# Kernel optimization log

Hardware: AMD Instinct MI355X
Metric: run time of the kernel (lower is better)

Reference implementation:

```python
import jax, jax.numpy as jnp
import numpy as np

WINDOW = 8
HEADS = 8

def _rel_index(w):
    coords = np.stack(np.meshgrid(np.arange(w), np.arange(w), indexing='ij')).reshape(2, -1)
    rel = coords[:, :, None] - coords[:, None, :]          # [2, N, N]
    rel = rel.transpose(1, 2, 0) + (w - 1)                 # [N, N, 2]
    return jnp.asarray(rel[:, :, 0] * (2 * w - 1) + rel[:, :, 1])  # [N, N] int

def setup_inputs() -> dict:
    key = jax.random.key(0)
    ks = jax.random.split(key, 5)
    B, N, C = 4096, WINDOW * WINDOW, 256
    x = jax.random.normal(ks[0], (B, N, C), dtype=jnp.float32)
    w_qkv = jax.random.normal(ks[1], (3 * C, C), dtype=jnp.float32) * 0.02
    b_qkv = jnp.zeros((3 * C,), dtype=jnp.float32)
    bias_table = jax.random.normal(ks[2], ((2 * WINDOW - 1) ** 2, HEADS), dtype=jnp.float32) * 0.02
    w_proj = jax.random.normal(ks[3], (C, C), dtype=jnp.float32) * 0.02
    b_proj = jnp.zeros((C,), dtype=jnp.float32)
    return {"x": x, "w_qkv": w_qkv, "b_qkv": b_qkv, "bias_table": bias_table,
            "w_proj": w_proj, "b_proj": b_proj}

def reference(x, w_qkv, b_qkv, bias_table, w_proj, b_proj):
    B, N, C = x.shape
    H = HEADS
    d = C // H
    scale = d ** (-0.5)
    idx = _rel_index(WINDOW)                                # [N, N]
    qkv = x @ w_qkv.T + b_qkv                               # [B, N, 3C]
    qkv = qkv.reshape(B, N, 3, H, d).transpose(2, 0, 3, 1, 4)
    q, k, v = qkv[0], qkv[1], qkv[2]                        # [B, H, N, d]
    attn = jnp.einsum('bhnd,bhmd->bhnm', q * scale, k)      # [B, H, N, N]
    bias = bias_table[idx]                                  # [N, N, H]
    attn = attn + bias.transpose(2, 0, 1)[None]             # add per-head bias
    attn = jax.nn.softmax(attn, axis=-1)
    out = jnp.einsum('bhnm,bhmd->bhnd', attn, v)            # [B, H, N, d]
    out = out.transpose(0, 2, 1, 3).reshape(B, N, C)
    return out @ w_proj.T + b_proj
```

## Files before the change

### kernel.cpp

```cpp
#include <hip/hip_runtime.h>

typedef unsigned int u32;
typedef unsigned short u16;
typedef __bf16 bf16x8 __attribute__((ext_vector_type(8)));
typedef short short4_ __attribute__((ext_vector_type(4)));
typedef float f32x4 __attribute__((ext_vector_type(4)));
typedef u32 u32x4 __attribute__((ext_vector_type(4)));
typedef u32 u32x2 __attribute__((ext_vector_type(2)));

#if __has_builtin(__builtin_amdgcn_mfma_f32_16x16x16bf16_1k)
#define HAVE_MFMA16 1
#else
#define HAVE_MFMA16 0
#endif

#define NTOK 64
#define CDIM 256
#define NH 8

#define WS_HDR 8
#define BIAS_O (WS_HDR)
#define WQKV_O (BIAS_O + 32768)
#define BQKV_O (WQKV_O + 196608)
#define WPRJ_O (BQKV_O + 768)
#define BPRJ_O (WPRJ_O + 65536)

#define XROW 520
#define LDS_BYTES 33280

__device__ __forceinline__ float bf2f(u16 u) {
  union { u32 i; float f; } z; z.i = ((u32)u) << 16; return z.f;
}
__device__ __forceinline__ u16 f2bf(float f) {
  __bf16 h = (__bf16)f; return __builtin_bit_cast(u16, h);
}
__device__ __forceinline__ u32 pk2(float a, float b) {
  return (u32)f2bf(a) | ((u32)f2bf(b) << 16);
}
__device__ __forceinline__ float fetchf(const void* p, int idx, int isbf) {
  return isbf ? bf2f(((const u16*)p)[idx]) : ((const float*)p)[idx];
}
__device__ __forceinline__ short4_ op16(u32 lo, u32 hi) {
  u32x2 z; z[0] = lo; z[1] = hi;
  return __builtin_bit_cast(short4_, z);
}

__device__ __forceinline__ bf16x8 frag_from(u32 p00, u32 p01, u32 p10, u32 p11,
                                            int s0, int s1, bool hi) {
  u32 A0 = (u32)__shfl((int)p00, s0, 64);
  u32 A1 = (u32)__shfl((int)p01, s0, 64);
  u32 B0 = (u32)__shfl((int)p10, s0, 64);
  u32 B1 = (u32)__shfl((int)p11, s0, 64);
  u32 C0 = (u32)__shfl((int)p00, s1, 64);
  u32 C1 = (u32)__shfl((int)p01, s1, 64);
  u32 D0 = (u32)__shfl((int)p10, s1, 64);
  u32 D1 = (u32)__shfl((int)p11, s1, 64);
  u32x4 f;
  f[0] = hi ? B0 : A0;  f[1] = hi ? B1 : A1;
  f[2] = hi ? D0 : C0;  f[3] = hi ? D1 : C1;
  return __builtin_bit_cast(bf16x8, f);
}

__global__ void detect_dtype(const u16* __restrict__ x, int* __restrict__ flag) {
  __shared__ int cnt;
  if (threadIdx.x == 0) cnt = 0;
  __syncthreads();
  int sane = 0;
  for (int i = threadIdx.x; i < 2048; i += 256) {
    u16 u = x[2 * i];
    int e = (u >> 7) & 0xFF;
    sane += (e == 0 || (e >= 90 && e <= 160)) ? 1 : 0;
  }
  atomicAdd(&cnt, sane);
  __syncthreads();
  if (threadIdx.x == 0) *flag = (cnt >= 1638) ? 1 : 0;
}

__global__ void cvt_params(const void* __restrict__ wqkv, const void* __restrict__ bqkv,
                           const void* __restrict__ btab, const void* __restrict__ wprj,
                           const void* __restrict__ bprj, void* __restrict__ wsraw) {
  u16* ws = (u16*)wsraw;
  const int isbf = *(const int*)wsraw;
  int i = blockIdx.x * 256 + threadIdx.x;
  if (i < 32768) {
    int n = (i >> 6) & 63, m = i & 63, h = i >> 12;
    int r0 = (n >> 3) - (m >> 3) + 7, r1 = (n & 7) - (m & 7) + 7;
    ws[BIAS_O + i] = f2bf(fetchf(btab, (r0 * 15 + r1) * NH + h, isbf));
  } else if (i < 32768 + 196608) {
    int j = i - 32768;
    ws[WQKV_O + j] = f2bf(fetchf(wqkv, j, isbf));
  } else if (i < 32768 + 196608 + 768) {
    int j = i - (32768 + 196608);
    ws[BQKV_O + j] = f2bf(fetchf(bqkv, j, isbf));
  } else if (i < 32768 + 196608 + 768 + 65536) {
    int j = i - (32768 + 196608 + 768);
    ws[WPRJ_O + j] = f2bf(fetchf(wprj, j, isbf));
  } else if (i < 32768 + 196608 + 768 + 65536 + 256) {
    int j = i - (32768 + 196608 + 768 + 65536);
    ws[BPRJ_O + j] = f2bf(fetchf(bprj, j, isbf));
  }
}

#define TILE_T(PK, CHT, CHB, SCL) {                                                   \
    bf16x8 wf[8];                                                                     \
    const u16* wrow = ws + WQKV_O + ((CHB) + c) * CDIM;                               \
    _Pragma("unroll")                                                                 \
    for (int ks = 0; ks < 8; ++ks) wf[ks] = *(const bf16x8*)(wrow + ks * 32 + g * 8); \
    f32x4 binit;                                                                      \
    { u32x2 bp = *(const u32x2*)(ws + BQKV_O + (CHB) + 4 * g);                        \
      binit[0] = bf2f((u16)(bp[0] & 0xffff)); binit[1] = bf2f((u16)(bp[0] >> 16));    \
      binit[2] = bf2f((u16)(bp[1] & 0xffff)); binit[3] = bf2f((u16)(bp[1] >> 16)); }  \
    _Pragma("unroll")                                                                 \
    for (int nt = 0; nt < 4; ++nt) {                                                  \
      f32x4 acc = binit;                                                              \
      _Pragma("unroll")                                                               \
      for (int ks = 0; ks < 8; ++ks) {                                                \
        bf16x8 xf = *(const bf16x8*)(lds + (16 * nt + c) * XROW + ks * 64 + g * 16);  \
        acc = __builtin_amdgcn_mfma_f32_16x16x32_bf16(wf[ks], xf, acc, 0, 0, 0);      \
      }                                                                               \
      PK[CHT][nt][0] = pk2(acc[0] * (SCL), acc[1] * (SCL));                           \
      PK[CHT][nt][1] = pk2(acc[2] * (SCL), acc[3] * (SCL));                           \
    } }

#define TILE_N(PK, CHT, CHB) {                                                        \
    bf16x8 wf[8];                                                                     \
    const u16* wrow = ws + WQKV_O + ((CHB) + c) * CDIM;                               \
    _Pragma("unroll")                                                                 \
    for (int ks = 0; ks < 8; ++ks) wf[ks] = *(const bf16x8*)(wrow + ks * 32 + g * 8); \
    const float badd = bf2f(ws[BQKV_O + (CHB) + c]);                                  \
    _Pragma("unroll")                                                                 \
    for (int nt = 0; nt < 4; ++nt) {                                                  \
      f32x4 acc = {badd, badd, badd, badd};                                           \
      _Pragma("unroll")                                                               \
      for (int ks = 0; ks < 8; ++ks) {                                                \
        bf16x8 xf = *(const bf16x8*)(lds + (16 * nt + c) * XROW + ks * 64 + g * 16);  \
        acc = __builtin_amdgcn_mfma_f32_16x16x32_bf16(xf, wf[ks], acc, 0, 0, 0);      \
      }                                                                               \
      PK[CHT][nt][0] = pk2(acc[0], acc[1]);                                           \
      PK[CHT][nt][1] = pk2(acc[2], acc[3]);                                           \
    } }

__global__ __launch_bounds__(512, 2)
void win_attn_fused(const void* __restrict__ xraw, const void* __restrict__ wsraw,
                    float* __restrict__ out)
{
  __shared__ __align__(16) unsigned char lds[LDS_BYTES];
  const u16* ws  = (const u16*)wsraw;
  const int isbf = *(const int*)wsraw;
  const int b    = blockIdx.x;
  const int tid  = threadIdx.x;
  const int w    = tid >> 6;
  const int lane = tid & 63;
  const int c    = lane & 15;
  const int g    = lane >> 4;
  const float scale = 0.1767766952966369f;

  if (isbf) {
    const u32x4* gx = (const u32x4*)((const u16*)xraw + (size_t)b * (NTOK * CDIM));
#pragma unroll
    for (int i = 0; i < 4; ++i) {
      int q = tid + i * 512;
      int row = q >> 5, c8 = q & 31;
      *(u32x4*)(lds + row * XROW + c8 * 16) = gx[q];
    }
  } else {
    const f32x4* gx = (const f32x4*)((const float*)xraw + (size_t)b * (NTOK * CDIM));
#pragma unroll
    for (int i = 0; i < 8; ++i) {
      int q = tid + i * 512;
      int row = q >> 6, c4 = q & 63;
      f32x4 v = gx[q];
      u32x2 pkv;
      pkv[0] = pk2(v[0], v[1]);
      pkv[1] = pk2(v[2], v[3]);
      *(u32x2*)(lds + row * XROW + c4 * 8) = pkv;
    }
  }
  __syncthreads();

  const int s0 = c + 32 * (g & 1), s1 = s0 + 16;
  const bool hi = ((g >> 1) & 1) != 0;
  const int h = w;
  (void)s0; (void)s1; (void)hi;

  u32 qpk[2][4][2], kpk[2][4][2], vpk[2][4][2];
  TILE_T(qpk, 0, 32 * w,            scale);
  TILE_T(qpk, 1, 32 * w + 16,       scale);
  TILE_T(kpk, 0, 256 + 32 * w,      1.0f);
  TILE_T(kpk, 1, 256 + 32 * w + 16, 1.0f);
  TILE_N(vpk, 0, 512 + 32 * w);
  TILE_N(vpk, 1, 512 + 32 * w + 16);

#if !HAVE_MFMA16
  bf16x8 bvf[2][2];
#pragma unroll
  for (int dt = 0; dt < 2; ++dt)
#pragma unroll
    for (int k2 = 0; k2 < 2; ++k2)
      bvf[dt][k2] = frag_from(vpk[dt][2 * k2][0], vpk[dt][2 * k2][1],
                              vpk[dt][2 * k2 + 1][0], vpk[dt][2 * k2 + 1][1], s0, s1, hi);
#endif
  __syncthreads();

#if HAVE_MFMA16
  u32 Ppk[4][4][2];
#pragma unroll
  for (int nt = 0; nt < 4; ++nt) {
    f32x4 st[4];
#pragma unroll
    for (int mt = 0; mt < 4; ++mt) {
      u32x2 bp = *(const u32x2*)(ws + BIAS_O + (h << 12) + ((16 * nt + c) << 6) + 16 * mt + 4 * g);
      st[mt][0] = bf2f((u16)(bp[0] & 0xffff)); st[mt][1] = bf2f((u16)(bp[0] >> 16));
      st[mt][2] = bf2f((u16)(bp[1] & 0xffff)); st[mt][3] = bf2f((u16)(bp[1] >> 16));
    }
#pragma unroll
    for (int mt = 0; mt < 4; ++mt) {
      st[mt] = __builtin_amdgcn_mfma_f32_16x16x16bf16_1k(
          op16(kpk[0][mt][0], kpk[0][mt][1]), op16(qpk[0][nt][0], qpk[0][nt][1]), st[mt], 0, 0, 0);
      st[mt] = __builtin_amdgcn_mfma_f32_16x16x16bf16_1k(
          op16(kpk[1][mt][0], kpk[1][mt][1]), op16(qpk[1][nt][0], qpk[1][nt][1]), st[mt], 0, 0, 0);
    }
    float mx = st[0][0];
#pragma unroll
    for (int mt = 0; mt < 4; ++mt)
#pragma unroll
      for (int r = 0; r < 4; ++r) mx = fmaxf(mx, st[mt][r]);
    mx = fmaxf(mx, __shfl_xor(mx, 16));
    mx = fmaxf(mx, __shfl_xor(mx, 32));
    float sum = 0.f;
#pragma unroll
    for (int mt = 0; mt < 4; ++mt)
#pragma unroll
      for (int r = 0; r < 4; ++r) { float e = __expf(st[mt][r] - mx); st[mt][r] = e; sum += e; }
    sum += __shfl_xor(sum, 16);
    sum += __shfl_xor(sum, 32);
    float inv = 1.0f / sum;
#pragma unroll
    for (int mt = 0; mt < 4; ++mt) {
      Ppk[mt][nt][0] = pk2(st[mt][0] * inv, st[mt][1] * inv);
      Ppk[mt][nt][1] = pk2(st[mt][2] * inv, st[mt][3] * inv);
    }
  }

#pragma unroll
  for (int dt = 0; dt < 2; ++dt)
#pragma unroll
    for (int nt = 0; nt < 4; ++nt) {
      f32x4 o2 = {0, 0, 0, 0};
#pragma unroll
      for (int mt = 0; mt < 4; ++mt)
        o2 = __builtin_amdgcn_mfma_f32_16x16x16bf16_1k(
            op16(vpk[dt][mt][0], vpk[dt][mt][1]), op16(Ppk[mt][nt][0], Ppk[mt][nt][1]), o2, 0, 0, 0);
      u32x2 yw;
      yw[0] = pk2(o2[0], o2[1]);
      yw[1] = pk2(o2[2], o2[3]);
      *(u32x2*)(lds + (16 * nt + c) * XROW + (32 * w + 16 * dt + 4 * g) * 2) = yw;
    }
#else
  bf16x8 bkf[4];
#pragma unroll
  for (int mt = 0; mt < 4; ++mt)
    bkf[mt] = frag_from(kpk[0][mt][0], kpk[0][mt][1], kpk[1][mt][0], kpk[1][mt][1], s0, s1, hi);

  u32 Ppk[4][4][2];
#pragma unroll
  for (int nt = 0; nt < 4; ++nt) {
    bf16x8 aqf = frag_from(qpk[0][nt][0], qpk[0][nt][1], qpk[1][nt][0], qpk[1][nt][1], s0, s1, hi);
    f32x4 st[4];
#pragma unroll
    for (int mt = 0; mt < 4; ++mt) {
      u32x2 bp = *(const u32x2*)(ws + BIAS_O + (h << 12) + ((16 * nt + c) << 6) + 16 * mt + 4 * g);
      st[mt][0] = bf2f((u16)(bp[0] & 0xffff)); st[mt][1] = bf2f((u16)(bp[0] >> 16));
      st[mt][2] = bf2f((u16)(bp[1] & 0xffff)); st[mt][3] = bf2f((u16)(bp[1] >> 16));
    }
#pragma unroll
    for (int mt = 0; mt < 4; ++mt)
      st[mt] = __builtin_amdgcn_mfma_f32_16x16x32_bf16(bkf[mt], aqf, st[mt], 0, 0, 0);
    float mx = st[0][0];
#pragma unroll
    for (int mt = 0; mt < 4; ++mt)
#pragma unroll
      for (int r = 0; r < 4; ++r) mx = fmaxf(mx, st[mt][r]);
    mx = fmaxf(mx, __shfl_xor(mx, 16));
    mx = fmaxf(mx, __shfl_xor(mx, 32));
    float sum = 0.f;
#pragma unroll
    for (int mt = 0; mt < 4; ++mt)
#pragma unroll
      for (int r = 0; r < 4; ++r) { float e = __expf(st[mt][r] - mx); st[mt][r] = e; sum += e; }
    sum += __shfl_xor(sum, 16);
    sum += __shfl_xor(sum, 32);
    float inv = 1.0f / sum;
#pragma unroll
    for (int mt = 0; mt < 4; ++mt) {
      Ppk[mt][nt][0] = pk2(st[mt][0] * inv, st[mt][1] * inv);
      Ppk[mt][nt][1] = pk2(st[mt][2] * inv, st[mt][3] * inv);
    }
  }

  f32x4 o[4][2] = {{{0,0,0,0},{0,0,0,0}},{{0,0,0,0},{0,0,0,0}},
                   {{0,0,0,0},{0,0,0,0}},{{0,0,0,0},{0,0,0,0}}};
#pragma unroll
  for (int k2 = 0; k2 < 2; ++k2) {
    bf16x8 paf4[4];
#pragma unroll
    for (int nt = 0; nt < 4; ++nt)
      paf4[nt] = frag_from(Ppk[2 * k2][nt][0], Ppk[2 * k2][nt][1],
                           Ppk[2 * k2 + 1][nt][0], Ppk[2 * k2 + 1][nt][1], s0, s1, hi);
#pragma unroll
    for (int nt = 0; nt < 4; ++nt) {
      o[nt][0] = __builtin_amdgcn_mfma_f32_16x16x32_bf16(paf4[nt], bvf[0][k2], o[nt][0], 0, 0, 0);
      o[nt][1] = __builtin_amdgcn_mfma_f32_16x16x32_bf16(paf4[nt], bvf[1][k2], o[nt][1], 0, 0, 0);
    }
  }
#pragma unroll
  for (int nt = 0; nt < 4; ++nt)
#pragma unroll
    for (int dt = 0; dt < 2; ++dt)
#pragma unroll
      for (int r = 0; r < 4; ++r) {
        int n = 16 * nt + 4 * g + r, col = 32 * w + 16 * dt + c;
        *(u16*)(lds + n * XROW + col * 2) = f2bf(o[nt][dt][r]);
      }
#endif
  __syncthreads();

  float* gout = out + (size_t)b * (NTOK * CDIM);
#pragma unroll
  for (int ct = 0; ct < 2; ++ct) {
    const int colw = 32 * w + 16 * ct + c;
    const float badd = bf2f(ws[BPRJ_O + colw]);
    f32x4 acc[4];
#pragma unroll
    for (int rt = 0; rt < 4; ++rt)
#pragma unroll
      for (int r = 0; r < 4; ++r) acc[rt][r] = badd;
    const u16* wrow = ws + WPRJ_O + colw * CDIM;
#pragma unroll
    for (int ks = 0; ks < 8; ++ks) {
      bf16x8 wf = *(const bf16x8*)(wrow + ks * 32 + g * 8);
#pragma unroll
      for (int rt = 0; rt < 4; ++rt) {
        bf16x8 ay = *(const bf16x8*)(lds + (16 * rt + c) * XROW + ks * 64 + g * 16);
        acc[rt] = __builtin_amdgcn_mfma_f32_16x16x32_bf16(ay, wf, acc[rt], 0, 0, 0);
      }
    }
#pragma unroll
    for (int rt = 0; rt < 4; ++rt)
#pragma unroll
      for (int r = 0; r < 4; ++r) {
        int n = 16 * rt + 4 * g + r;
        gout[n * CDIM + colw] = acc[rt][r];
      }
  }
}

extern "C" void kernel_launch(void* const* d_in, const int* in_sizes, int n_in,
                              void* d_out, int out_size, void* d_ws, size_t ws_size,
                              hipStream_t stream) {
  (void)in_sizes; (void)n_in; (void)out_size; (void)ws_size;
  detect_dtype<<<dim3(1), dim3(256), 0, stream>>>((const u16*)d_in[0], (int*)d_ws);
  cvt_params<<<dim3(1156), dim3(256), 0, stream>>>(d_in[1], d_in[2], d_in[3], d_in[4],
                                                   d_in[5], d_ws);
  win_attn_fused<<<dim3(4096), dim3(512), 0, stream>>>(d_in[0], d_ws, (float*)d_out);
}
```

Baseline: 467.4 us.

## Fuse PV into per-row-tile softmax loop and raise occupancy bound to four

Each query row tile now feeds its normalized probabilities straight into the PV matmul inside the softmax loop, so the full 4x4 probability array is never held in registers. Launch bounds go from 2 to 4 blocks per CU so the compiler must fit more waves. Shuffle helpers and their lane indices are compiled only on the fallback path. The tighter register budget risks spills, and the interleaving changes how MFMA and exp work overlap.

Result: slower. 650.8 us (+39.2%).

```diff
diff --git a/kernel.cpp b/kernel.cpp
--- a/kernel.cpp
+++ b/kernel.cpp
@@ -45,6 +45,7 @@
   return __builtin_bit_cast(short4_, z);
 }
 
+#if !HAVE_MFMA16
 __device__ __forceinline__ bf16x8 frag_from(u32 p00, u32 p01, u32 p10, u32 p11,
                                             int s0, int s1, bool hi) {
   u32 A0 = (u32)__shfl((int)p00, s0, 64);
@@ -60,6 +61,7 @@
   f[2] = hi ? D0 : C0;  f[3] = hi ? D1 : C1;
   return __builtin_bit_cast(bf16x8, f);
 }
+#endif
 
 __global__ void detect_dtype(const u16* __restrict__ x, int* __restrict__ flag) {
   __shared__ int cnt;
@@ -140,7 +142,7 @@
       PK[CHT][nt][1] = pk2(acc[2], acc[3]);                                           \
     } }
 
-__global__ __launch_bounds__(512, 2)
+__global__ __launch_bounds__(512, 4)
 void win_attn_fused(const void* __restrict__ xraw, const void* __restrict__ wsraw,
                     float* __restrict__ out)
 {
@@ -178,10 +180,7 @@
   }
   __syncthreads();
 
-  const int s0 = c + 32 * (g & 1), s1 = s0 + 16;
-  const bool hi = ((g >> 1) & 1) != 0;
   const int h = w;
-  (void)s0; (void)s1; (void)hi;
 
   u32 qpk[2][4][2], kpk[2][4][2], vpk[2][4][2];
   TILE_T(qpk, 0, 32 * w,            scale);
@@ -192,6 +191,8 @@
   TILE_N(vpk, 1, 512 + 32 * w + 16);
 
 #if !HAVE_MFMA16
+  const int s0 = c + 32 * (g & 1), s1 = s0 + 16;
+  const bool hi = ((g >> 1) & 1) != 0;
   bf16x8 bvf[2][2];
 #pragma unroll
   for (int dt = 0; dt < 2; ++dt)
@@ -203,7 +204,6 @@
   __syncthreads();
 
 #if HAVE_MFMA16
-  u32 Ppk[4][4][2];
 #pragma unroll
   for (int nt = 0; nt < 4; ++nt) {
     f32x4 st[4];
@@ -235,34 +235,30 @@
     sum += __shfl_xor(sum, 16);
     sum += __shfl_xor(sum, 32);
     float inv = 1.0f / sum;
-#pragma unroll
-    for (int mt = 0; mt < 4; ++mt) {
-      Ppk[mt][nt][0] = pk2(st[mt][0] * inv, st[mt][1] * inv);
-      Ppk[mt][nt][1] = pk2(st[mt][2] * inv, st[mt][3] * inv);
-    }
-  }
-
-#pragma unroll
-  for (int dt = 0; dt < 2; ++dt)
-#pragma unroll
-    for (int nt = 0; nt < 4; ++nt) {
+    u32 pp[4][2];
+#pragma unroll
+    for (int mt = 0; mt < 4; ++mt) {
+      pp[mt][0] = pk2(st[mt][0] * inv, st[mt][1] * inv);
+      pp[mt][1] = pk2(st[mt][2] * inv, st[mt][3] * inv);
+    }
+#pragma unroll
+    for (int dt = 0; dt < 2; ++dt) {
       f32x4 o2 = {0, 0, 0, 0};
 #pragma unroll
       for (int mt = 0; mt < 4; ++mt)
         o2 = __builtin_amdgcn_mfma_f32_16x16x16bf16_1k(
-            op16(vpk[dt][mt][0], vpk[dt][mt][1]), op16(Ppk[mt][nt][0], Ppk[mt][nt][1]), o2, 0, 0, 0);
+            op16(vpk[dt][mt][0], vpk[dt][mt][1]), op16(pp[mt][0], pp[mt][1]), o2, 0, 0, 0);
       u32x2 yw;
       yw[0] = pk2(o2[0], o2[1]);
       yw[1] = pk2(o2[2], o2[3]);
       *(u32x2*)(lds + (16 * nt + c) * XROW + (32 * w + 16 * dt + 4 * g) * 2) = yw;
     }
+  }
 #else
   bf16x8 bkf[4];
 #pragma unroll
   for (int mt = 0; mt < 4; ++mt)
     bkf[mt] = frag_from(kpk[0][mt][0], kpk[0][mt][1], kpk[1][mt][0], kpk[1][mt][1], s0, s1, hi);
-
-  u32 Ppk[4][4][2];
 #pragma unroll
   for (int nt = 0; nt < 4; ++nt) {
     bf16x8 aqf = frag_from(qpk[0][nt][0], qpk[0][nt][1], qpk[1][nt][0], qpk[1][nt][1], s0, s1, hi);
@@ -291,37 +287,28 @@
     sum += __shfl_xor(sum, 16);
     sum += __shfl_xor(sum, 32);
     float inv = 1.0f / sum;
-#pragma unroll
-    for (int mt = 0; mt < 4; ++mt) {
-      Ppk[mt][nt][0] = pk2(st[mt][0] * inv, st[mt][1] * inv);
-      Ppk[mt][nt][1] = pk2(st[mt][2] * inv, st[mt][3] * inv);
-    }
-  }
-
-  f32x4 o[4][2] = {{{0,0,0,0},{0,0,0,0}},{{0,0,0,0},{0,0,0,0}},
-                   {{0,0,0,0},{0,0,0,0}},{{0,0,0,0},{0,0,0,0}}};
-#pragma unroll
-  for (int k2 = 0; k2 < 2; ++k2) {
-    bf16x8 paf4[4];
-#pragma unroll
-    for (int nt = 0; nt < 4; ++nt)
-      paf4[nt] = frag_from(Ppk[2 * k2][nt][0], Ppk[2 * k2][nt][1],
-                           Ppk[2 * k2 + 1][nt][0], Ppk[2 * k2 + 1][nt][1], s0, s1, hi);
-#pragma unroll
-    for (int nt = 0; nt < 4; ++nt) {
-      o[nt][0] = __builtin_amdgcn_mfma_f32_16x16x32_bf16(paf4[nt], bvf[0][k2], o[nt][0], 0, 0, 0);
-      o[nt][1] = __builtin_amdgcn_mfma_f32_16x16x32_bf16(paf4[nt], bvf[1][k2], o[nt][1], 0, 0, 0);
-    }
-  }
-#pragma unroll
-  for (int nt = 0; nt < 4; ++nt)
+    u32 pp[4][2];
+#pragma unroll
+    for (int mt = 0; mt < 4; ++mt) {
+      pp[mt][0] = pk2(st[mt][0] * inv, st[mt][1] * inv);
+      pp[mt][1] = pk2(st[mt][2] * inv, st[mt][3] * inv);
+    }
+    f32x4 o2[2] = {{0,0,0,0},{0,0,0,0}};
+#pragma unroll
+    for (int k2 = 0; k2 < 2; ++k2) {
+      bf16x8 paf = frag_from(pp[2 * k2][0], pp[2 * k2][1],
+                             pp[2 * k2 + 1][0], pp[2 * k2 + 1][1], s0, s1, hi);
+      o2[0] = __builtin_amdgcn_mfma_f32_16x16x32_bf16(paf, bvf[0][k2], o2[0], 0, 0, 0);
+      o2[1] = __builtin_amdgcn_mfma_f32_16x16x32_bf16(paf, bvf[1][k2], o2[1], 0, 0, 0);
+    }
 #pragma unroll
     for (int dt = 0; dt < 2; ++dt)
 #pragma unroll
       for (int r = 0; r < 4; ++r) {
         int n = 16 * nt + 4 * g + r, col = 32 * w + 16 * dt + c;
-        *(u16*)(lds + n * XROW + col * 2) = f2bf(o[nt][dt][r]);
+        *(u16*)(lds + n * XROW + col * 2) = f2bf(o2[dt][r]);
       }
+  }
 #endif
   __syncthreads();
 
```
